# Kernel optimization log

Hardware: AMD Instinct MI355X
Metric: run time of the kernel (lower is better)

The kernel has to match this reference:

```python
import jax, jax.numpy as jnp
import numpy as np

T, H, B = 1024, 512, 64

def setup_inputs() -> dict:
    key = jax.random.key(0)
    ks = jax.random.split(key, 9)
    s = 1.0 / np.sqrt(H)
    inp = {"in_seq": jax.random.normal(ks[0], (T, H, B), dtype=jnp.float32)}
    for i, name in enumerate(["Wxi", "Wxf", "Wxo", "Wxg", "Whi", "Whf", "Who", "Whg"]):
        inp[name] = jax.random.normal(ks[i + 1], (H, H), dtype=jnp.float32) * s
    return inp


def reference(in_seq, Wxi, Wxf, Wxo, Wxg, Whi, Whf, Who, Whg):
    # in_seq: [T, H, B]; x_t, h_t, c_t: [H, B]
    h0 = jnp.zeros_like(in_seq[0])
    c0 = jnp.zeros_like(in_seq[0])

    def step(carry, x):
        h, c = carry
        i = jax.nn.sigmoid(Wxi @ x + Whi @ h)
        f = jax.nn.sigmoid(Wxf @ x + Whf @ h)
        g = jnp.tanh(Wxg @ x + Whg @ h)
        o = jax.nn.sigmoid(Wxo @ x + Who @ h)
        c = f * c + i * g
        h = o * jnp.tanh(c)
        return (h, c), h

    (h, c), outputs = jax.lax.scan(step, (h0, c0), in_seq)
    return outputs, h, c  # outputs: [T, H, B]
```

## Files before the change

kernel.cpp:

```cpp
#include <hip/hip_runtime.h>
#include <hip/hip_bf16.h>

typedef unsigned short u16;
typedef unsigned int   u32;
typedef unsigned long long u64;

typedef __attribute__((ext_vector_type(8))) short short8;
typedef __attribute__((ext_vector_type(4))) float f32x4;
typedef __attribute__((ext_vector_type(4))) u32   u32x4;

#define TT 1024
#define HH 512
#define BB 64
#define GCOLS 8
#define NRB 32
#define LDSK 536

#define HTB_PAR 16384
#define HTB_GRP 2048
#define HTB_WORDS (2 * HTB_PAR)

__device__ __forceinline__ u16 f2bf(float f) {
    union { float f; u32 u; } v; v.f = f;
    u32 u = v.u;
    return (u16)((u + 0x7FFFu + ((u >> 16) & 1u)) >> 16);
}

__device__ __forceinline__ short8 cvt8(const float4 &a, const float4 &b) {
    short8 r;
    r[0] = (short)f2bf(a.x); r[1] = (short)f2bf(a.y);
    r[2] = (short)f2bf(a.z); r[3] = (short)f2bf(a.w);
    r[4] = (short)f2bf(b.x); r[5] = (short)f2bf(b.y);
    r[6] = (short)f2bf(b.z); r[7] = (short)f2bf(b.w);
    return r;
}

__device__ __forceinline__ float fast_rcp(float x) {
    float r; asm("v_rcp_f32 %0, %1" : "=v"(r) : "v"(x)); return r;
}
__device__ __forceinline__ float fast_sigmoid(float x) {
    return fast_rcp(1.f + __expf(-x));
}
__device__ __forceinline__ float fast_tanh(float x) {
    float e = __expf(2.f * x);
    return 1.f - 2.f * fast_rcp(e + 1.f);
}

__device__ __forceinline__ void load4_l2(const u64* p, u32x4 &A, u32x4 &B, u32x4 &C, u32x4 &D) {
    asm volatile(
        "global_load_dwordx4 %0, %4, off sc0\n\t"
        "global_load_dwordx4 %1, %4, off offset:16 sc0\n\t"
        "global_load_dwordx4 %2, %4, off offset:32 sc0\n\t"
        "global_load_dwordx4 %3, %4, off offset:48 sc0\n\t"
        "s_waitcnt vmcnt(0)"
        : "=v"(A), "=v"(B), "=v"(C), "=v"(D) : "v"(p) : "memory");
}
__device__ __forceinline__ void load4_llc(const u64* p, u32x4 &A, u32x4 &B, u32x4 &C, u32x4 &D) {
    asm volatile(
        "global_load_dwordx4 %0, %4, off sc0 sc1\n\t"
        "global_load_dwordx4 %1, %4, off offset:16 sc0 sc1\n\t"
        "global_load_dwordx4 %2, %4, off offset:32 sc0 sc1\n\t"
        "global_load_dwordx4 %3, %4, off offset:48 sc0 sc1\n\t"
        "s_waitcnt vmcnt(0)"
        : "=v"(A), "=v"(B), "=v"(C), "=v"(D) : "v"(p) : "memory");
}
__device__ __forceinline__ void store_l2(u64* p, u64 v) {
    asm volatile("global_store_dwordx2 %0, %1, off" :: "v"(p), "v"(v) : "memory");
}
__device__ __forceinline__ void store_llc(u64* p, u64 v) {
    asm volatile("global_store_dwordx2 %0, %1, off sc0 sc1" :: "v"(p), "v"(v) : "memory");
}

__global__ __launch_bounds__(256, 1)
void lstm_persist(const float* __restrict__ in_seq,
                  const float* __restrict__ Wxi, const float* __restrict__ Wxf,
                  const float* __restrict__ Wxo, const float* __restrict__ Wxg,
                  const float* __restrict__ Whi, const float* __restrict__ Whf,
                  const float* __restrict__ Who, const float* __restrict__ Whg,
                  float* __restrict__ out, u64* htbC, u64* htb2)
{
    __shared__ u16 xt[2][16][LDSK];
    __shared__ u16 htl[16][LDSK];
    __shared__ float gates[4][16][8];

    const int tid  = threadIdx.x;
    const int bid  = blockIdx.x;
    const int g    = bid & 7;
    const int rblk = bid >> 3;
    const int wave = tid >> 6;
    const int lane = tid & 63;
    const int lrow = lane & 15;
    const int lk8  = (lane >> 4) * 8;

    {
        u16* p0 = &xt[0][0][0]; u16* p1 = &htl[0][0];
        for (int i = tid; i < 2 * 16 * LDSK; i += 256) p0[i] = 0;
        for (int i = tid; i < 16 * LDSK; i += 256) p1[i] = 0;
    }

    const float* Wx = (wave == 0) ? Wxi : (wave == 1) ? Wxf : (wave == 2) ? Wxo : Wxg;
    const float* Wh = (wave == 0) ? Whi : (wave == 1) ? Whf : (wave == 2) ? Who : Whg;

    short8 afrag[32];
    const int grow = rblk * 16 + lrow;
    #pragma unroll
    for (int kk = 0; kk < 16; ++kk) {
        const float* s = Wx + grow * HH + kk * 32 + lk8;
        afrag[kk] = cvt8(*(const float4*)s, *(const float4*)(s + 4));
    }
    #pragma unroll
    for (int kk = 0; kk < 16; ++kk) {
        const float* s = Wh + grow * HH + kk * 32 + lk8;
        afrag[16 + kk] = cvt8(*(const float4*)s, *(const float4*)(s + 4));
    }

    float cst = 0.f;
    const int hr  = (tid & 127) >> 3;
    const int col = tid & 7;
    const int hid = rblk * 16 + hr;

    const int sc   = tid >> 5;
    const int sk0  = (tid & 31) * 16;
    const int soff = g * HTB_GRP + sc * 256 + (tid & 31) * 8;
    const int doff = g * HTB_GRP + col * 256 + (hid >> 1);

    bool llc_mode = false;
    int  failruns = 0;

    float4 a0, a1, b0, b1;
    {
        const float* xb = in_seq + (size_t)(tid * 2) * BB + g * GCOLS;
        a0 = *(const float4*)(xb);      a1 = *(const float4*)(xb + 4);
        b0 = *(const float4*)(xb + BB); b1 = *(const float4*)(xb + BB + 4);
        int k = tid * 2;
        const float *ra = (const float*)&a0, *rb = (const float*)&b0;
        #pragma unroll
        for (int j = 0; j < 4; ++j)
            *(u32*)&xt[0][j][k] = (u32)f2bf(ra[j]) | ((u32)f2bf(rb[j]) << 16);
        const float *ra1 = (const float*)&a1, *rb1 = (const float*)&b1;
        #pragma unroll
        for (int j = 0; j < 4; ++j)
            *(u32*)&xt[0][4 + j][k] = (u32)f2bf(ra1[j]) | ((u32)f2bf(rb1[j]) << 16);
    }
    __syncthreads();

    for (int t = 0; t < TT; ++t) {
        f32x4 acc = {0.f, 0.f, 0.f, 0.f};
        {
            const u16 (*xc)[LDSK] = xt[t & 1];
            #pragma unroll
            for (int kk = 0; kk < 16; ++kk) {
                short8 bfr = *(const short8*)&xc[lrow][kk * 32 + lk8];
                acc = __builtin_amdgcn_mfma_f32_16x16x32_bf16(afrag[kk], bfr, acc, 0, 0, 0);
            }
        }

        if (t > 0) {
            const u64* p2 = htb2 + (t & 1) * HTB_PAR + soff;
            const u64* pC = htbC + (t & 1) * HTB_PAR + soff;
            const u32 want = (u32)t;
            u32x4 A, B, C, D;
            bool got = false;
            if (!llc_mode) {
                for (int r = 0; r < 6 && !got; ++r) {
                    load4_l2(p2, A, B, C, D);
                    got = (A[1] == want) & (A[3] == want) & (B[1] == want) & (B[3] == want) &
                          (C[1] == want) & (C[3] == want) & (D[1] == want) & (D[3] == want);
                }
            }
            if (!got) {
                do {
                    load4_llc(pC, A, B, C, D);
                    got = (A[1] == want) & (A[3] == want) & (B[1] == want) & (B[3] == want) &
                          (C[1] == want) & (C[3] == want) & (D[1] == want) & (D[3] == want);
                } while (!got);
                if (t > 32 && ++failruns >= 3) llc_mode = true;
            } else {
                failruns = 0;
            }
            u32x4 lo, hi;
            lo[0] = A[0]; lo[1] = A[2]; lo[2] = B[0]; lo[3] = B[2];
            hi[0] = C[0]; hi[1] = C[2]; hi[2] = D[0]; hi[3] = D[2];
            *(u32x4*)&htl[sc][sk0]     = lo;
            *(u32x4*)&htl[sc][sk0 + 8] = hi;
        }

        if (t + 1 < TT) {
            const float* xb = in_seq + (size_t)(t + 1) * (HH * BB)
                            + (size_t)(tid * 2) * BB + g * GCOLS;
            a0 = *(const float4*)(xb);      a1 = *(const float4*)(xb + 4);
            b0 = *(const float4*)(xb + BB); b1 = *(const float4*)(xb + BB + 4);
        }
        __syncthreads();

        #pragma unroll
        for (int kk = 0; kk < 16; ++kk) {
            short8 bfr = *(const short8*)&htl[lrow][kk * 32 + lk8];
            acc = __builtin_amdgcn_mfma_f32_16x16x32_bf16(afrag[16 + kk], bfr, acc, 0, 0, 0);
        }
        if (lrow < 8) {
            #pragma unroll
            for (int r = 0; r < 4; ++r)
                gates[wave][(lane >> 4) * 4 + r][lrow] = acc[r];
        }
        __syncthreads();

        if (tid < 128) {
            float ip = gates[0][hr][col];
            float fp = gates[1][hr][col];
            float op = gates[2][hr][col];
            float gp = gates[3][hr][col];
            float iv = fast_sigmoid(ip);
            float fv = fast_sigmoid(fp);
            float ov = fast_sigmoid(op);
            float gv = fast_tanh(gp);
            cst = fv * cst + iv * gv;
            float hv = ov * fast_tanh(cst);
            out[(size_t)t * (HH * BB) + hid * BB + g * GCOLS + col] = hv;

            u16 hb16 = f2bf(hv);
            u32 up = (u32)__shfl_down((int)(u32)hb16, 8);
            if ((hr & 1) == 0) {
                u64 pack = ((u64)(u32)(t + 1) << 32) | ((u64)(up & 0xffffu) << 16) | (u64)hb16;
                int off = ((t + 1) & 1) * HTB_PAR + doff;
                store_l2(htb2 + off, pack);
                store_llc(htbC + off, pack);
            }
            if (t == TT - 1) {
                size_t base = (size_t)TT * HH * BB;
                out[base + hid * BB + g * GCOLS + col] = hv;
                out[base + HH * BB + hid * BB + g * GCOLS + col] = cst;
            }
        }

        if (t + 1 < TT) {
            int k = tid * 2;
            u16 (*xn)[LDSK] = xt[(t + 1) & 1];
            const float *ra = (const float*)&a0, *rb = (const float*)&b0;
            #pragma unroll
            for (int j = 0; j < 4; ++j)
                *(u32*)&xn[j][k] = (u32)f2bf(ra[j]) | ((u32)f2bf(rb[j]) << 16);
            const float *ra1 = (const float*)&a1, *rb1 = (const float*)&b1;
            #pragma unroll
            for (int j = 0; j < 4; ++j)
                *(u32*)&xn[4 + j][k] = (u32)f2bf(ra1[j]) | ((u32)f2bf(rb1[j]) << 16);
        }
        __syncthreads();
    }
}

extern "C" void kernel_launch(void* const* d_in, const int* in_sizes, int n_in,
                              void* d_out, int out_size, void* d_ws, size_t ws_size,
                              hipStream_t stream)
{
    const float* in_seq = (const float*)d_in[0];
    const float* Wxi = (const float*)d_in[1];
    const float* Wxf = (const float*)d_in[2];
    const float* Wxo = (const float*)d_in[3];
    const float* Wxg = (const float*)d_in[4];
    const float* Whi = (const float*)d_in[5];
    const float* Whf = (const float*)d_in[6];
    const float* Who = (const float*)d_in[7];
    const float* Whg = (const float*)d_in[8];

    u64* htbC = (u64*)d_ws;
    u64* htb2 = (u64*)d_ws + HTB_WORDS;

    lstm_persist<<<256, 256, 0, stream>>>(in_seq, Wxi, Wxf, Wxo, Wxg,
                                          Whi, Whf, Who, Whg,
                                          (float*)d_out, htbC, htb2);
}
```

Measured before the change: 2.308 ms.

## Interleave gate rows per wave to fuse LSTM cell update in registers

Weight rows are redistributed so each wave's MFMA tile holds all four gates (i,f,o,g) for four hidden units. The gate values then land in one lane's accumulator, so the cell update runs directly from registers, which removes the gates LDS buffer and one __syncthreads per timestep. The MFMA chains are also split into two independent accumulators each to shorten dependency latency. LDS row padding and the L2 polling and LLC fallback thresholds are retuned as well.

```diff
diff --git a/kernel.cpp b/kernel.cpp
--- a/kernel.cpp
+++ b/kernel.cpp
@@ -13,8 +13,7 @@
 #define HH 512
 #define BB 64
 #define GCOLS 8
-#define NRB 32
-#define LDSK 536
+#define LDSK 528
 
 #define HTB_PAR 16384
 #define HTB_GRP 2048
@@ -81,7 +80,6 @@
 {
     __shared__ u16 xt[2][16][LDSK];
     __shared__ u16 htl[16][LDSK];
-    __shared__ float gates[4][16][8];
 
     const int tid  = threadIdx.x;
     const int bid  = blockIdx.x;
@@ -98,34 +96,35 @@
         for (int i = tid; i < 16 * LDSK; i += 256) p1[i] = 0;
     }
 
-    const float* Wx = (wave == 0) ? Wxi : (wave == 1) ? Wxf : (wave == 2) ? Wxo : Wxg;
-    const float* Wh = (wave == 0) ? Whi : (wave == 1) ? Whf : (wave == 2) ? Who : Whg;
+    const int gt   = lrow & 3;
+    const int grow = rblk * 16 + wave * 4 + (lrow >> 2);
+    const float* WxS = (gt == 0) ? Wxi : (gt == 1) ? Wxf : (gt == 2) ? Wxo : Wxg;
+    const float* WhS = (gt == 0) ? Whi : (gt == 1) ? Whf : (gt == 2) ? Who : Whg;
 
     short8 afrag[32];
-    const int grow = rblk * 16 + lrow;
     #pragma unroll
     for (int kk = 0; kk < 16; ++kk) {
-        const float* s = Wx + grow * HH + kk * 32 + lk8;
+        const float* s = WxS + grow * HH + kk * 32 + lk8;
         afrag[kk] = cvt8(*(const float4*)s, *(const float4*)(s + 4));
     }
     #pragma unroll
     for (int kk = 0; kk < 16; ++kk) {
-        const float* s = Wh + grow * HH + kk * 32 + lk8;
+        const float* s = WhS + grow * HH + kk * 32 + lk8;
         afrag[16 + kk] = cvt8(*(const float4*)s, *(const float4*)(s + 4));
     }
 
+    const int q    = lane >> 4;
+    const int colv = lrow;
+    const int hid  = rblk * 16 + wave * 4 + q;
     float cst = 0.f;
-    const int hr  = (tid & 127) >> 3;
-    const int col = tid & 7;
-    const int hid = rblk * 16 + hr;
 
     const int sc   = tid >> 5;
     const int sk0  = (tid & 31) * 16;
     const int soff = g * HTB_GRP + sc * 256 + (tid & 31) * 8;
-    const int doff = g * HTB_GRP + col * 256 + (hid >> 1);
-
-    bool llc_mode = false;
-    int  failruns = 0;
+    const int doff = g * HTB_GRP + colv * 256 + (hid >> 1);
+
+    int  fail_steps = 0;
+    bool llc_mode   = false;
 
     float4 a0, a1, b0, b1;
     {
@@ -145,13 +144,18 @@
     __syncthreads();
 
     for (int t = 0; t < TT; ++t) {
-        f32x4 acc = {0.f, 0.f, 0.f, 0.f};
+        f32x4 aA = {0.f, 0.f, 0.f, 0.f}, aB = {0.f, 0.f, 0.f, 0.f};
         {
             const u16 (*xc)[LDSK] = xt[t & 1];
             #pragma unroll
-            for (int kk = 0; kk < 16; ++kk) {
+            for (int kk = 0; kk < 8; ++kk) {
                 short8 bfr = *(const short8*)&xc[lrow][kk * 32 + lk8];
-                acc = __builtin_amdgcn_mfma_f32_16x16x32_bf16(afrag[kk], bfr, acc, 0, 0, 0);
+                aA = __builtin_amdgcn_mfma_f32_16x16x32_bf16(afrag[kk], bfr, aA, 0, 0, 0);
+            }
+            #pragma unroll
+            for (int kk = 8; kk < 16; ++kk) {
+                short8 bfr = *(const short8*)&xc[lrow][kk * 32 + lk8];
+                aB = __builtin_amdgcn_mfma_f32_16x16x32_bf16(afrag[kk], bfr, aB, 0, 0, 0);
             }
         }
 
@@ -162,7 +166,7 @@
             u32x4 A, B, C, D;
             bool got = false;
             if (!llc_mode) {
-                for (int r = 0; r < 6 && !got; ++r) {
+                for (int r = 0; r < 16 && !got; ++r) {
                     load4_l2(p2, A, B, C, D);
                     got = (A[1] == want) & (A[3] == want) & (B[1] == want) & (B[3] == want) &
                           (C[1] == want) & (C[3] == want) & (D[1] == want) & (D[3] == want);
@@ -174,9 +178,9 @@
                     got = (A[1] == want) & (A[3] == want) & (B[1] == want) & (B[3] == want) &
                           (C[1] == want) & (C[3] == want) & (D[1] == want) & (D[3] == want);
                 } while (!got);
-                if (t > 32 && ++failruns >= 3) llc_mode = true;
+                if (++fail_steps >= 8 && t > 16) llc_mode = true;
             } else {
-                failruns = 0;
+                fail_steps = 0;
             }
             u32x4 lo, hi;
             lo[0] = A[0]; lo[1] = A[2]; lo[2] = B[0]; lo[3] = B[2];
@@ -193,43 +197,40 @@
         }
         __syncthreads();
 
-        #pragma unroll
-        for (int kk = 0; kk < 16; ++kk) {
+        f32x4 aC = {0.f, 0.f, 0.f, 0.f}, aD = {0.f, 0.f, 0.f, 0.f};
+        #pragma unroll
+        for (int kk = 0; kk < 8; ++kk) {
             short8 bfr = *(const short8*)&htl[lrow][kk * 32 + lk8];
-            acc = __builtin_amdgcn_mfma_f32_16x16x32_bf16(afrag[16 + kk], bfr, acc, 0, 0, 0);
-        }
-        if (lrow < 8) {
-            #pragma unroll
-            for (int r = 0; r < 4; ++r)
-                gates[wave][(lane >> 4) * 4 + r][lrow] = acc[r];
-        }
-        __syncthreads();
-
-        if (tid < 128) {
-            float ip = gates[0][hr][col];
-            float fp = gates[1][hr][col];
-            float op = gates[2][hr][col];
-            float gp = gates[3][hr][col];
-            float iv = fast_sigmoid(ip);
-            float fv = fast_sigmoid(fp);
-            float ov = fast_sigmoid(op);
-            float gv = fast_tanh(gp);
+            aC = __builtin_amdgcn_mfma_f32_16x16x32_bf16(afrag[16 + kk], bfr, aC, 0, 0, 0);
+        }
+        #pragma unroll
+        for (int kk = 8; kk < 16; ++kk) {
+            short8 bfr = *(const short8*)&htl[lrow][kk * 32 + lk8];
+            aD = __builtin_amdgcn_mfma_f32_16x16x32_bf16(afrag[16 + kk], bfr, aD, 0, 0, 0);
+        }
+        f32x4 acc = (aA + aB) + (aC + aD);
+
+        if (colv < 8) {
+            float iv = fast_sigmoid(acc[0]);
+            float fv = fast_sigmoid(acc[1]);
+            float ov = fast_sigmoid(acc[2]);
+            float gv = fast_tanh(acc[3]);
             cst = fv * cst + iv * gv;
             float hv = ov * fast_tanh(cst);
-            out[(size_t)t * (HH * BB) + hid * BB + g * GCOLS + col] = hv;
-
-            u16 hb16 = f2bf(hv);
-            u32 up = (u32)__shfl_down((int)(u32)hb16, 8);
-            if ((hr & 1) == 0) {
-                u64 pack = ((u64)(u32)(t + 1) << 32) | ((u64)(up & 0xffffu) << 16) | (u64)hb16;
+
+            u16 hb = f2bf(hv);
+            u32 up = (u32)__shfl_down((int)(u32)hb, 16);
+            if ((q & 1) == 0) {
+                u64 pack = ((u64)(u32)(t + 1) << 32) | ((u64)(up & 0xffffu) << 16) | (u64)hb;
                 int off = ((t + 1) & 1) * HTB_PAR + doff;
                 store_l2(htb2 + off, pack);
                 store_llc(htbC + off, pack);
             }
+            out[(size_t)t * (HH * BB) + hid * BB + g * GCOLS + colv] = hv;
             if (t == TT - 1) {
                 size_t base = (size_t)TT * HH * BB;
-                out[base + hid * BB + g * GCOLS + col] = hv;
-                out[base + HH * BB + hid * BB + g * GCOLS + col] = cst;
+                out[base + hid * BB + g * GCOLS + colv] = hv;
+                out[base + HH * BB + hid * BB + g * GCOLS + colv] = cst;
             }
         }
 
```

Measured after the change: 2.947 ms. +27.7%, slower.
